# Optimization experiments

Hardware: AMD Instinct MI355X
Metric: run time of the kernel (lower is better)

Reference implementation:

```python
import jax, jax.numpy as jnp
import numpy as np
import math

N_HEAD = 16


def _alibi_slopes(n_head):
    def get_slopes(n):
        start = 2.0 ** (-2.0 ** (-(math.log2(n) - 3)))
        return [start * start ** i for i in range(n)]
    if math.log2(n_head).is_integer():
        slopes = get_slopes(n_head)
    else:
        c = 2 ** math.floor(math.log2(n_head))
        slopes = get_slopes(c)
        extra = get_slopes(2 * c)[0::2]
        slopes = slopes + extra[: n_head - c]
    return np.asarray(slopes, dtype=np.float32)


def setup_inputs() -> dict:
    key = jax.random.key(0)
    ks = jax.random.split(key, 9)
    B, S, E = 2, 2048, 1024
    sd = 1.0 / math.sqrt(E)
    inp = {
        "x": jax.random.normal(ks[0], (B, S, E), jnp.float32),
        "Wq": jax.random.uniform(ks[1], (E, E), jnp.float32, -sd, sd),
        "bq": jnp.zeros((E,), jnp.float32),
        "Wk": jax.random.uniform(ks[2], (E, E), jnp.float32, -sd, sd),
        "bk": jnp.zeros((E,), jnp.float32),
        "Wv": jax.random.uniform(ks[3], (E, E), jnp.float32, -sd, sd),
        "bv": jnp.zeros((E,), jnp.float32),
        "Wo": jax.random.uniform(ks[4], (E, E), jnp.float32, -sd, sd),
        "bo": jnp.zeros((E,), jnp.float32),
        "alibi_slopes": jnp.asarray(_alibi_slopes(N_HEAD)),
    }
    return inp


def reference(x, Wq, bq, Wk, bk, Wv, bv, Wo, bo, alibi_slopes):
    B, S, E = x.shape
    H = N_HEAD
    hd = E // H
    scale = hd ** -0.5
    # Linear layers (torch Linear: y = x @ W.T + b)
    Q = (x @ Wq.T + bq).reshape(B, H, S, hd)  # faithful: view, NOT transpose
    K = (x @ Wk.T + bk).reshape(B, H, S, hd)
    V = (x @ Wv.T + bv).reshape(B, H, S, hd)
    scores = jnp.einsum("bhqd,bhkd->bhqk", Q, K) * scale
    pos = jnp.arange(S)
    rel = jnp.abs(pos[None, :] - pos[:, None]).astype(scores.dtype)  # [S,S]
    bias = alibi_slopes[None, :, None, None] * rel[None, None]  # [1,H,S,S]
    scores = scores - bias
    probs = jax.nn.softmax(scores, axis=-1)
    # faithful quirk: keep only head index 1's probs, broadcast to all heads
    probs1 = probs[:, 1:2, :, :]  # [B,1,S,S]
    attn_out = jnp.matmul(probs1, V)  # broadcast -> [B,H,S,hd]
    attn_out = attn_out.reshape(B, S, E)
    out = attn_out @ Wo.T + bo
    return (out, probs1)
```

## Files before the change

### kernel.cpp

```cpp
#include <hip/hip_runtime.h>

typedef __bf16 bf16;
typedef __bf16 bf16_4 __attribute__((ext_vector_type(4)));
typedef __bf16 bf16_8 __attribute__((ext_vector_type(8)));
typedef float f32_4 __attribute__((ext_vector_type(4)));

#define GLDS16(g, l) \
  __builtin_amdgcn_global_load_lds((const __attribute__((address_space(1))) unsigned int*)(g), \
                                   (__attribute__((address_space(3))) unsigned int*)(l), 16, 0, 0)

__global__ __launch_bounds__(256) void convert_all(
    const float* __restrict__ x, const float* __restrict__ wq, const float* __restrict__ wk,
    const float* __restrict__ wv, const float* __restrict__ wo,
    bf16* __restrict__ xb, bf16* __restrict__ wqb, bf16* __restrict__ wkb,
    bf16* __restrict__ wvb, bf16* __restrict__ wob)
{
    for (int i = blockIdx.x * 256 + threadIdx.x; i < 2097152; i += 2048 * 256) {
        const float* s; bf16* d; int off;
        if (i < 1048576) { s = x; d = xb; off = i; }
        else {
            int j = i - 1048576;
            int sel = j >> 18;
            off = j & 262143;
            s = (sel == 0) ? wq : (sel == 1) ? wk : (sel == 2) ? wv : wo;
            d = (sel == 0) ? wqb : (sel == 1) ? wkb : (sel == 2) ? wvb : wob;
        }
        float4 v = reinterpret_cast<const float4*>(s)[off];
        bf16_4 o; o.x = (bf16)v.x; o.y = (bf16)v.y; o.z = (bf16)v.z; o.w = (bf16)v.w;
        reinterpret_cast<bf16_4*>(d)[off] = o;
    }
}

template<int BM, int KU>
__device__ __forceinline__ void gemm_core(
    const bf16* __restrict__ Ab, int lda,
    const bf16* __restrict__ Wb, int ldw,
    int K, int m0, int n0, int tid,
    bf16* As, bf16* Bs,
    f32_4 (&acc)[4][(BM == 128) ? 4 : 2])
{
    constexpr int NJ = (BM == 128) ? 4 : 2;
    constexpr int CA = BM * 8;
    const int lane = tid & 63;
    const int wave = tid >> 6;
    const int l15  = lane & 15;
    const int quad = lane >> 4;
    const int WM = (BM == 128) ? (wave >> 1) * 64 : 0;
    const int WN = (BM == 128) ? (wave & 1) * 64 : wave * 32;

#pragma unroll
    for (int i = 0; i < 4; i++)
#pragma unroll
        for (int j = 0; j < NJ; j++) acc[i][j] = (f32_4)(0.0f);

    for (int k0 = 0; k0 < K; k0 += 64 * KU) {
#pragma unroll
        for (int ku = 0; ku < KU; ++ku) {
            bf16* Asu = As + ku * BM * 64;
            bf16* Bsu = Bs + ku * 128 * 64;
            int kk = k0 + ku * 64;
#pragma unroll
            for (int it = 0; it < CA / 256; ++it) {
                int p = wave * (CA / 4) + it * 64 + lane;
                int r = p >> 3;
                int q = (p & 7) ^ (r & 7);
                GLDS16(Ab + (long long)(m0 + r) * lda + kk + q * 8, Asu + p * 8);
            }
#pragma unroll
            for (int it = 0; it < 4; ++it) {
                int p = wave * 256 + it * 64 + lane;
                int r = p >> 3;
                int q = (p & 7) ^ (r & 7);
                GLDS16(Wb + (long long)(n0 + r) * ldw + kk + q * 8, Bsu + p * 8);
            }
        }
        __syncthreads();

#pragma unroll
        for (int ku = 0; ku < KU; ++ku) {
            bf16* Asu = As + ku * BM * 64;
            bf16* Bsu = Bs + ku * 128 * 64;
#pragma unroll
            for (int kh = 0; kh < 2; ++kh) {
                bf16_8 af[4], bfr[NJ];
#pragma unroll
                for (int t = 0; t < 4; ++t) {
                    int r = WM + t * 16 + l15;
                    int q = (kh * 4 + quad) ^ (r & 7);
                    af[t] = *reinterpret_cast<const bf16_8*>(&Asu[r * 64 + q * 8]);
                }
#pragma unroll
                for (int j = 0; j < NJ; ++j) {
                    int r = WN + j * 16 + l15;
                    int q = (kh * 4 + quad) ^ (r & 7);
                    bfr[j] = *reinterpret_cast<const bf16_8*>(&Bsu[r * 64 + q * 8]);
                }
#pragma unroll
                for (int i = 0; i < 4; ++i)
#pragma unroll
                    for (int j = 0; j < NJ; ++j)
                        acc[i][j] = __builtin_amdgcn_mfma_f32_16x16x32_bf16(af[i], bfr[j], acc[i][j], 0, 0, 0);
            }
        }
        __syncthreads();
    }
}

__global__ __launch_bounds__(256) void proj_merged(
    const bf16* __restrict__ x_bf,
    const bf16* __restrict__ wv_bf, const float* __restrict__ bv, bf16* __restrict__ v_bf,
    const bf16* __restrict__ wq_bf, const float* __restrict__ bq, bf16* __restrict__ qh1,
    const bf16* __restrict__ wk_bf, const float* __restrict__ bk, bf16* __restrict__ kh1)
{
    __shared__ alignas(16) bf16 As[64 * 64 * 2];
    __shared__ alignas(16) bf16 Bs[128 * 64 * 2];
    const int tid = threadIdx.x;
    const int lane = tid & 63, wave = tid >> 6, l15 = lane & 15, quad = lane >> 4;
    const int n0 = blockIdx.x * 128;

    int m0;
    const bf16* Ab; const bf16* Wb; const float* bvec; bf16* op;
    long long obase;
    int y = blockIdx.y;
    if (y < 64) { m0 = y * 64; Ab = x_bf; Wb = wv_bf; bvec = bv; op = v_bf; obase = 0; }
    else {
        int sub = y - 64;
        int batch = (sub >> 1) & 1;
        int sel = sub >> 2;
        m0 = (sub & 1) * 64;
        Ab = x_bf + (long long)batch * 2097152LL + 131072LL;
        Wb = sel ? wk_bf : wq_bf;
        bvec = sel ? bk : bq;
        op = sel ? kh1 : qh1;
        obase = (long long)batch * 131072LL;
    }

    f32_4 acc[4][2];
    gemm_core<64, 2>(Ab, 1024, Wb, 1024, 1024, m0, n0, tid, As, Bs, acc);

    const int WN = wave * 32;
#pragma unroll
    for (int i = 0; i < 4; i++)
#pragma unroll
        for (int j = 0; j < 2; j++)
#pragma unroll
            for (int rg = 0; rg < 4; rg++) {
                int m = m0 + i * 16 + quad * 4 + rg;
                int n = n0 + WN + j * 16 + l15;
                op[obase + (long long)m * 1024 + n] = (bf16)(acc[i][j][rg] + bvec[n]);
            }
}

__global__ __launch_bounds__(256) void scores_tr(
    const bf16* __restrict__ qh1, const bf16* __restrict__ kh1,
    const float* __restrict__ slopes,
    bf16* __restrict__ pb, float* __restrict__ spart,
    const unsigned short* __restrict__ v_bf, unsigned short* __restrict__ vt)
{
    __shared__ alignas(16) char smem[32768];
    bf16* As = (bf16*)smem;
    bf16* Bs = (bf16*)(smem + 16384);
    const int tid = threadIdx.x;
    const int lane = tid & 63, wave = tid >> 6, l15 = lane & 15, quad = lane >> 4;
    const int n0 = blockIdx.x * 128;
    const int m0 = blockIdx.y * 128;
    const int z  = blockIdx.z;

    f32_4 acc[4][4];
    gemm_core<128, 1>(qh1 + (long long)z * 131072LL, 64,
                      kh1 + (long long)z * 131072LL, 64, 64, m0, n0, tid, As, Bs, acc);

    const int WM = (wave >> 1) * 64;
    const int WN = (wave & 1) * 64;
    const float slope = slopes[1];
    long long obase = (long long)z * 4194304LL;
#pragma unroll
    for (int i = 0; i < 4; i++) {
#pragma unroll
        for (int rg = 0; rg < 4; rg++) {
            int m = m0 + WM + i * 16 + quad * 4 + rg;
            float rowpart = 0.0f;
#pragma unroll
            for (int j = 0; j < 4; j++) {
                int n = n0 + WN + j * 16 + l15;
                float v = acc[i][j][rg] * 0.125f - slope * fabsf((float)(m - n));
                float e = __expf(v);
                rowpart += e;
                pb[obase + (long long)m * 2048 + n] = (bf16)e;
            }
            rowpart += __shfl_xor(rowpart, 1, 64);
            rowpart += __shfl_xor(rowpart, 2, 64);
            rowpart += __shfl_xor(rowpart, 4, 64);
            rowpart += __shfl_xor(rowpart, 8, 64);
            if (l15 == 0)
                spart[((long long)z * 2048 + m) * 32 + (n0 >> 6) + (WN >> 6)] = rowpart;
        }
    }

    unsigned short* tile = (unsigned short*)smem;
    int flat = z * 256 + blockIdx.y * 16 + blockIdx.x;
#pragma unroll
    for (int uu = 0; uu < 2; ++uu) {
        int u = flat * 2 + uu;
        int k0 = (u & 31) * 64, h = (u >> 5) & 15, b = u >> 9;
        const unsigned short* src = v_bf + (long long)b * 2097152LL + (long long)h * 131072LL;
#pragma unroll
        for (int p = 0; p < 8; p++) {
            int idx = tid + p * 256;
            int k = idx >> 5, dc = idx & 31;
            ushort2 w = *reinterpret_cast<const ushort2*>(&src[(long long)(k0 + k) * 64 + dc * 2]);
            tile[(dc * 2) * 66 + k]     = w.x;
            tile[(dc * 2 + 1) * 66 + k] = w.y;
        }
        __syncthreads();
        unsigned short* dst = vt + (long long)b * 2097152LL + (long long)h * 64 * 2048LL + k0;
#pragma unroll
        for (int p = 0; p < 8; p++) {
            int idx = tid + p * 256;
            int d = idx >> 5, kc = idx & 31;
            ushort2 w;
            w.x = tile[d * 66 + kc * 2];
            w.y = tile[d * 66 + kc * 2 + 1];
            *reinterpret_cast<ushort2*>(&dst[(long long)d * 2048 + kc * 2]) = w;
        }
        __syncthreads();
    }
}

__global__ __launch_bounds__(256) void pv_fused(
    const bf16* __restrict__ pb, const bf16* __restrict__ vt,
    const float* __restrict__ spart,
    bf16* __restrict__ attn, float* __restrict__ probs_f)
{
    __shared__ alignas(16) bf16 As[64 * 64 * 2];
    __shared__ alignas(16) bf16 Bs[128 * 64 * 2];
    __shared__ float rs[64];
    const int tid = threadIdx.x;
    const int lane = tid & 63, wave = tid >> 6, l15 = lane & 15, quad = lane >> 4;
    const int nx = blockIdx.x;
    const int n0 = nx * 128;
    const int m0 = blockIdx.y * 64;
    const int z  = blockIdx.z;

    {
        int r = tid >> 2, part = tid & 3;
        const float* sp = spart + ((long long)z * 2048 + m0 + r) * 32 + part * 8;
        float4 a = *reinterpret_cast<const float4*>(sp);
        float4 b = *reinterpret_cast<const float4*>(sp + 4);
        float v = a.x + a.y + a.z + a.w + b.x + b.y + b.z + b.w;
        v += __shfl_xor(v, 1, 64);
        v += __shfl_xor(v, 2, 64);
        if (part == 0) rs[r] = 1.0f / v;
    }
    __syncthreads();

    const bf16* Ab = pb + (long long)z * 4194304LL;
    const bf16* Wb = vt + (long long)z * 2097152LL;

    f32_4 acc[4][2];
#pragma unroll
    for (int i = 0; i < 4; i++)
#pragma unroll
        for (int j = 0; j < 2; j++) acc[i][j] = (f32_4)(0.0f);

    for (int k0 = 0; k0 < 2048; k0 += 128) {
#pragma unroll
        for (int ku = 0; ku < 2; ++ku) {
            bf16* Asu = As + ku * 4096;
            bf16* Bsu = Bs + ku * 8192;
            int kk = k0 + ku * 64;
#pragma unroll
            for (int it = 0; it < 2; ++it) {
                int p = wave * 128 + it * 64 + lane;
                int r = p >> 3, q = (p & 7) ^ (r & 7);
                GLDS16(Ab + (long long)(m0 + r) * 2048 + kk + q * 8, Asu + p * 8);
            }
#pragma unroll
            for (int it = 0; it < 4; ++it) {
                int p = wave * 256 + it * 64 + lane;
                int r = p >> 3, q = (p & 7) ^ (r & 7);
                GLDS16(Wb + (long long)(n0 + r) * 2048 + kk + q * 8, Bsu + p * 8);
            }
        }
        __syncthreads();

#pragma unroll
        for (int ku = 0; ku < 2; ++ku) {
            int kk = k0 + ku * 64;
            if ((kk >> 8) == nx) {
                bf16* Asu = As + ku * 4096;
#pragma unroll
                for (int s0 = 0; s0 < 2; ++s0) {
                    int s = tid + s0 * 256;
                    int r = s >> 3, q = s & 7;
                    bf16_8 e = *reinterpret_cast<const bf16_8*>(&Asu[r * 64 + (q ^ (r & 7)) * 8]);
                    float inv = rs[r];
                    float4 o0, o1;
                    o0.x = (float)e[0] * inv; o0.y = (float)e[1] * inv;
                    o0.z = (float)e[2] * inv; o0.w = (float)e[3] * inv;
                    o1.x = (float)e[4] * inv; o1.y = (float)e[5] * inv;
                    o1.z = (float)e[6] * inv; o1.w = (float)e[7] * inv;
                    long long base = ((long long)z * 2048 + m0 + r) * 2048 + kk + q * 8;
                    *reinterpret_cast<float4*>(&probs_f[base])     = o0;
                    *reinterpret_cast<float4*>(&probs_f[base + 4]) = o1;
                }
            }
        }

#pragma unroll
        for (int ku = 0; ku < 2; ++ku) {
            bf16* Asu = As + ku * 4096;
            bf16* Bsu = Bs + ku * 8192;
#pragma unroll
            for (int kh = 0; kh < 2; ++kh) {
                bf16_8 af[4], bfr[2];
#pragma unroll
                for (int t = 0; t < 4; ++t) {
                    int r = t * 16 + l15;
                    int q = (kh * 4 + quad) ^ (r & 7);
                    af[t] = *reinterpret_cast<const bf16_8*>(&Asu[r * 64 + q * 8]);
                }
                const int WN = wave * 32;
#pragma unroll
                for (int j = 0; j < 2; ++j) {
                    int r = WN + j * 16 + l15;
                    int q = (kh * 4 + quad) ^ (r & 7);
                    bfr[j] = *reinterpret_cast<const bf16_8*>(&Bsu[r * 64 + q * 8]);
                }
#pragma unroll
                for (int i = 0; i < 4; ++i)
#pragma unroll
                    for (int j = 0; j < 2; ++j)
                        acc[i][j] = __builtin_amdgcn_mfma_f32_16x16x32_bf16(af[i], bfr[j], acc[i][j], 0, 0, 0);
            }
        }
        __syncthreads();
    }

    const int WN = wave * 32;
    long long obase = (long long)z * 2097152LL;
#pragma unroll
    for (int i = 0; i < 4; i++)
#pragma unroll
        for (int j = 0; j < 2; j++)
#pragma unroll
            for (int rg = 0; rg < 4; rg++) {
                int ml = i * 16 + quad * 4 + rg;
                int m = m0 + ml;
                int n = n0 + WN + j * 16 + l15;
                float v = acc[i][j][rg] * rs[ml];
                long long off = obase + ((long long)(n >> 6)) * 131072LL + (long long)m * 64 + (n & 63);
                attn[off] = (bf16)v;
            }
}

__global__ __launch_bounds__(256) void out_proj(
    const bf16* __restrict__ attn, const bf16* __restrict__ wo_bf,
    const float* __restrict__ bo, float* __restrict__ out_f)
{
    __shared__ alignas(16) bf16 As[64 * 64 * 2];
    __shared__ alignas(16) bf16 Bs[128 * 64 * 2];
    const int tid = threadIdx.x;
    const int lane = tid & 63, wave = tid >> 6, l15 = lane & 15, quad = lane >> 4;
    const int n0 = blockIdx.x * 128;
    const int m0 = blockIdx.y * 64;

    f32_4 acc[4][2];
    gemm_core<64, 2>(attn, 1024, wo_bf, 1024, 1024, m0, n0, tid, As, Bs, acc);

    const int WN = wave * 32;
#pragma unroll
    for (int i = 0; i < 4; i++)
#pragma unroll
        for (int j = 0; j < 2; j++)
#pragma unroll
            for (int rg = 0; rg < 4; rg++) {
                int m = m0 + i * 16 + quad * 4 + rg;
                int n = n0 + WN + j * 16 + l15;
                out_f[(long long)m * 1024 + n] = acc[i][j][rg] + bo[n];
            }
}

extern "C" void kernel_launch(void* const* d_in, const int* in_sizes, int n_in,
                              void* d_out, int out_size, void* d_ws, size_t ws_size,
                              hipStream_t stream) {
    const float* x      = (const float*)d_in[0];
    const float* Wq     = (const float*)d_in[1];
    const float* bq     = (const float*)d_in[2];
    const float* Wk     = (const float*)d_in[3];
    const float* bk     = (const float*)d_in[4];
    const float* Wv     = (const float*)d_in[5];
    const float* bv     = (const float*)d_in[6];
    const float* Wo     = (const float*)d_in[7];
    const float* bo     = (const float*)d_in[8];
    const float* slopes = (const float*)d_in[9];

    char* w = (char*)d_ws;
    bf16* x_bf  = (bf16*)w;  w += 4096LL * 1024 * 2;
    bf16* wq_bf = (bf16*)w;  w += 1024LL * 1024 * 2;
    bf16* wk_bf = (bf16*)w;  w += 1024LL * 1024 * 2;
    bf16* wv_bf = (bf16*)w;  w += 1024LL * 1024 * 2;
    bf16* wo_bf = (bf16*)w;  w += 1024LL * 1024 * 2;
    bf16* qh1   = (bf16*)w;  w += 2LL * 131072 * 2;
    bf16* kh1   = (bf16*)w;  w += 2LL * 131072 * 2;
    bf16* v_bf  = (bf16*)w;  w += 4096LL * 1024 * 2;
    bf16* vt    = (bf16*)w;  w += 2LL * 1024 * 2048 * 2;
    bf16* attn  = (bf16*)w;  w += 4096LL * 1024 * 2;
    bf16* pb    = (bf16*)w;  w += 2LL * 2048 * 2048 * 2;
    float* spart = (float*)w; w += 4096LL * 32 * 4;

    float* out_f   = (float*)d_out;
    float* probs_f = (float*)d_out + 4194304LL;

    convert_all<<<2048, 256, 0, stream>>>(x, Wq, Wk, Wv, Wo, x_bf, wq_bf, wk_bf, wv_bf, wo_bf);

    proj_merged<<<dim3(8, 72, 1), 256, 0, stream>>>(
        x_bf, wv_bf, bv, v_bf, wq_bf, bq, qh1, wk_bf, bk, kh1);

    scores_tr<<<dim3(16, 16, 2), 256, 0, stream>>>(
        qh1, kh1, slopes, pb, spart,
        (const unsigned short*)v_bf, (unsigned short*)vt);

    pv_fused<<<dim3(8, 32, 2), 256, 0, stream>>>(pb, vt, spart, attn, probs_f);

    out_proj<<<dim3(8, 64, 1), 256, 0, stream>>>(attn, wo_bf, bo, out_f);
}
```

Before: 177.0 us.

## Double-buffer and enlarge tiles to 128x128 in PV and output projection GEMMs

```diff
diff --git a/kernel.cpp b/kernel.cpp
--- a/kernel.cpp
+++ b/kernel.cpp
@@ -103,6 +103,60 @@
             }
         }
         __syncthreads();
+    }
+}
+
+__device__ __forceinline__ void stage128(
+    const bf16* __restrict__ Ab, long long lda,
+    const bf16* __restrict__ Wb, long long ldw,
+    int m0, int n0, int kk0, int wave, int lane,
+    bf16* Asb, bf16* Bsb)
+{
+#pragma unroll
+    for (int ku = 0; ku < 2; ++ku) {
+        bf16* Asu = Asb + ku * 8192;
+        bf16* Bsu = Bsb + ku * 8192;
+        int kk = kk0 + ku * 64;
+#pragma unroll
+        for (int it = 0; it < 4; ++it) {
+            int p = wave * 256 + it * 64 + lane;
+            int r = p >> 3, q = (p & 7) ^ (r & 7);
+            GLDS16(Ab + (long long)(m0 + r) * lda + kk + q * 8, Asu + p * 8);
+            GLDS16(Wb + (long long)(n0 + r) * ldw + kk + q * 8, Bsu + p * 8);
+        }
+    }
+}
+
+__device__ __forceinline__ void mma128(
+    const bf16* Asb, const bf16* Bsb,
+    int WM, int WN, int l15, int quad,
+    f32_4 (&acc)[4][4])
+{
+#pragma unroll
+    for (int ku = 0; ku < 2; ++ku) {
+        const bf16* Asu = Asb + ku * 8192;
+        const bf16* Bsu = Bsb + ku * 8192;
+#pragma unroll
+        for (int kh = 0; kh < 2; ++kh) {
+            bf16_8 af[4], bfr[4];
+#pragma unroll
+            for (int t = 0; t < 4; ++t) {
+                int r = WM + t * 16 + l15;
+                int q = (kh * 4 + quad) ^ (r & 7);
+                af[t] = *reinterpret_cast<const bf16_8*>(&Asu[r * 64 + q * 8]);
+            }
+#pragma unroll
+            for (int j = 0; j < 4; ++j) {
+                int r = WN + j * 16 + l15;
+                int q = (kh * 4 + quad) ^ (r & 7);
+                bfr[j] = *reinterpret_cast<const bf16_8*>(&Bsu[r * 64 + q * 8]);
+            }
+#pragma unroll
+            for (int i = 0; i < 4; ++i)
+#pragma unroll
+                for (int j = 0; j < 4; ++j)
+                    acc[i][j] = __builtin_amdgcn_mfma_f32_16x16x32_bf16(af[i], bfr[j], acc[i][j], 0, 0, 0);
+        }
     }
 }
 
@@ -232,65 +286,60 @@
     const float* __restrict__ spart,
     bf16* __restrict__ attn, float* __restrict__ probs_f)
 {
-    __shared__ alignas(16) bf16 As[64 * 64 * 2];
-    __shared__ alignas(16) bf16 Bs[128 * 64 * 2];
-    __shared__ float rs[64];
+    __shared__ alignas(16) bf16 As[2][16384];
+    __shared__ alignas(16) bf16 Bs[2][16384];
+    __shared__ float rs[128];
     const int tid = threadIdx.x;
     const int lane = tid & 63, wave = tid >> 6, l15 = lane & 15, quad = lane >> 4;
     const int nx = blockIdx.x;
     const int n0 = nx * 128;
-    const int m0 = blockIdx.y * 64;
+    const int m0 = blockIdx.y * 128;
     const int z  = blockIdx.z;
+    const int WM = (wave >> 1) * 64, WN = (wave & 1) * 64;
+
+    const bf16* Ab = pb + (long long)z * 4194304LL;
+    const bf16* Wb = vt + (long long)z * 2097152LL;
+
+    stage128(Ab, 2048, Wb, 2048, m0, n0, 0, wave, lane, &As[0][0], &Bs[0][0]);
 
     {
-        int r = tid >> 2, part = tid & 3;
-        const float* sp = spart + ((long long)z * 2048 + m0 + r) * 32 + part * 8;
+        int r = tid >> 1, part = tid & 1;
+        const float* sp = spart + ((long long)z * 2048 + m0 + r) * 32 + part * 16;
         float4 a = *reinterpret_cast<const float4*>(sp);
         float4 b = *reinterpret_cast<const float4*>(sp + 4);
-        float v = a.x + a.y + a.z + a.w + b.x + b.y + b.z + b.w;
+        float4 c = *reinterpret_cast<const float4*>(sp + 8);
+        float4 d = *reinterpret_cast<const float4*>(sp + 12);
+        float v = a.x + a.y + a.z + a.w + b.x + b.y + b.z + b.w
+                + c.x + c.y + c.z + c.w + d.x + d.y + d.z + d.w;
         v += __shfl_xor(v, 1, 64);
-        v += __shfl_xor(v, 2, 64);
         if (part == 0) rs[r] = 1.0f / v;
     }
     __syncthreads();
 
-    const bf16* Ab = pb + (long long)z * 4194304LL;
-    const bf16* Wb = vt + (long long)z * 2097152LL;
-
-    f32_4 acc[4][2];
-#pragma unroll
-    for (int i = 0; i < 4; i++)
-#pragma unroll
-        for (int j = 0; j < 2; j++) acc[i][j] = (f32_4)(0.0f);
-
-    for (int k0 = 0; k0 < 2048; k0 += 128) {
+    f32_4 acc[4][4];
+#pragma unroll
+    for (int i = 0; i < 4; i++)
+#pragma unroll
+        for (int j = 0; j < 4; j++) acc[i][j] = (f32_4)(0.0f);
+
+    for (int t = 0; t < 16; ++t) {
+        const int cur = t & 1;
+        if (t < 15) {
+            stage128(Ab, 2048, Wb, 2048, m0, n0, (t + 1) * 128, wave, lane,
+                     &As[cur ^ 1][0], &Bs[cur ^ 1][0]);
+            asm volatile("s_waitcnt vmcnt(16)" ::: "memory");
+        } else {
+            asm volatile("s_waitcnt vmcnt(0)" ::: "memory");
+        }
+        __builtin_amdgcn_s_barrier();
+
 #pragma unroll
         for (int ku = 0; ku < 2; ++ku) {
-            bf16* Asu = As + ku * 4096;
-            bf16* Bsu = Bs + ku * 8192;
-            int kk = k0 + ku * 64;
-#pragma unroll
-            for (int it = 0; it < 2; ++it) {
-                int p = wave * 128 + it * 64 + lane;
-                int r = p >> 3, q = (p & 7) ^ (r & 7);
-                GLDS16(Ab + (long long)(m0 + r) * 2048 + kk + q * 8, Asu + p * 8);
-            }
-#pragma unroll
-            for (int it = 0; it < 4; ++it) {
-                int p = wave * 256 + it * 64 + lane;
-                int r = p >> 3, q = (p & 7) ^ (r & 7);
-                GLDS16(Wb + (long long)(n0 + r) * 2048 + kk + q * 8, Bsu + p * 8);
-            }
-        }
-        __syncthreads();
-
-#pragma unroll
-        for (int ku = 0; ku < 2; ++ku) {
-            int kk = k0 + ku * 64;
+            int kk = t * 128 + ku * 64;
             if ((kk >> 8) == nx) {
-                bf16* Asu = As + ku * 4096;
-#pragma unroll
-                for (int s0 = 0; s0 < 2; ++s0) {
+                const bf16* Asu = &As[cur][ku * 8192];
+#pragma unroll
+                for (int s0 = 0; s0 < 4; ++s0) {
                     int s = tid + s0 * 256;
                     int r = s >> 3, q = s & 7;
                     bf16_8 e = *reinterpret_cast<const bf16_8*>(&Asu[r * 64 + (q ^ (r & 7)) * 8]);
@@ -307,45 +356,20 @@
             }
         }
 
-#pragma unroll
-        for (int ku = 0; ku < 2; ++ku) {
-            bf16* Asu = As + ku * 4096;
-            bf16* Bsu = Bs + ku * 8192;
-#pragma unroll
-            for (int kh = 0; kh < 2; ++kh) {
-                bf16_8 af[4], bfr[2];
-#pragma unroll
-                for (int t = 0; t < 4; ++t) {
-                    int r = t * 16 + l15;
-                    int q = (kh * 4 + quad) ^ (r & 7);
-                    af[t] = *reinterpret_cast<const bf16_8*>(&Asu[r * 64 + q * 8]);
-                }
-                const int WN = wave * 32;
-#pragma unroll
-                for (int j = 0; j < 2; ++j) {
-                    int r = WN + j * 16 + l15;
-                    int q = (kh * 4 + quad) ^ (r & 7);
-                    bfr[j] = *reinterpret_cast<const bf16_8*>(&Bsu[r * 64 + q * 8]);
-                }
-#pragma unroll
-                for (int i = 0; i < 4; ++i)
-#pragma unroll
-                    for (int j = 0; j < 2; ++j)
-                        acc[i][j] = __builtin_amdgcn_mfma_f32_16x16x32_bf16(af[i], bfr[j], acc[i][j], 0, 0, 0);
-            }
-        }
-        __syncthreads();
-    }
-
-    const int WN = wave * 32;
+        mma128(&As[cur][0], &Bs[cur][0], WM, WN, l15, quad, acc);
+
+        asm volatile("s_waitcnt lgkmcnt(0)" ::: "memory");
+        __builtin_amdgcn_s_barrier();
+    }
+
     long long obase = (long long)z * 2097152LL;
 #pragma unroll
     for (int i = 0; i < 4; i++)
 #pragma unroll
-        for (int j = 0; j < 2; j++)
+        for (int j = 0; j < 4; j++)
 #pragma unroll
             for (int rg = 0; rg < 4; rg++) {
-                int ml = i * 16 + quad * 4 + rg;
+                int ml = WM + i * 16 + quad * 4 + rg;
                 int m = m0 + ml;
                 int n = n0 + WN + j * 16 + l15;
                 float v = acc[i][j][rg] * rs[ml];
@@ -358,24 +382,47 @@
     const bf16* __restrict__ attn, const bf16* __restrict__ wo_bf,
     const float* __restrict__ bo, float* __restrict__ out_f)
 {
-    __shared__ alignas(16) bf16 As[64 * 64 * 2];
-    __shared__ alignas(16) bf16 Bs[128 * 64 * 2];
+    __shared__ alignas(16) bf16 As[2][16384];
+    __shared__ alignas(16) bf16 Bs[2][16384];
     const int tid = threadIdx.x;
     const int lane = tid & 63, wave = tid >> 6, l15 = lane & 15, quad = lane >> 4;
     const int n0 = blockIdx.x * 128;
-    const int m0 = blockIdx.y * 64;
-
-    f32_4 acc[4][2];
-    gemm_core<64, 2>(attn, 1024, wo_bf, 1024, 1024, m0, n0, tid, As, Bs, acc);
-
-    const int WN = wave * 32;
-#pragma unroll
-    for (int i = 0; i < 4; i++)
-#pragma unroll
-        for (int j = 0; j < 2; j++)
+    const int m0 = blockIdx.y * 128;
+    const int WM = (wave >> 1) * 64, WN = (wave & 1) * 64;
+
+    stage128(attn, 1024, wo_bf, 1024, m0, n0, 0, wave, lane, &As[0][0], &Bs[0][0]);
+    __syncthreads();
+
+    f32_4 acc[4][4];
+#pragma unroll
+    for (int i = 0; i < 4; i++)
+#pragma unroll
+        for (int j = 0; j < 4; j++) acc[i][j] = (f32_4)(0.0f);
+
+    for (int t = 0; t < 8; ++t) {
+        const int cur = t & 1;
+        if (t < 7) {
+            stage128(attn, 1024, wo_bf, 1024, m0, n0, (t + 1) * 128, wave, lane,
+                     &As[cur ^ 1][0], &Bs[cur ^ 1][0]);
+            asm volatile("s_waitcnt vmcnt(16)" ::: "memory");
+        } else {
+            asm volatile("s_waitcnt vmcnt(0)" ::: "memory");
+        }
+        __builtin_amdgcn_s_barrier();
+
+        mma128(&As[cur][0], &Bs[cur][0], WM, WN, l15, quad, acc);
+
+        asm volatile("s_waitcnt lgkmcnt(0)" ::: "memory");
+        __builtin_amdgcn_s_barrier();
+    }
+
+#pragma unroll
+    for (int i = 0; i < 4; i++)
+#pragma unroll
+        for (int j = 0; j < 4; j++)
 #pragma unroll
             for (int rg = 0; rg < 4; rg++) {
-                int m = m0 + i * 16 + quad * 4 + rg;
+                int m = m0 + WM + i * 16 + quad * 4 + rg;
                 int n = n0 + WN + j * 16 + l15;
                 out_f[(long long)m * 1024 + n] = acc[i][j][rg] + bo[n];
             }
@@ -421,7 +468,7 @@
         qh1, kh1, slopes, pb, spart,
         (const unsigned short*)v_bf, (unsigned short*)vt);
 
-    pv_fused<<<dim3(8, 32, 2), 256, 0, stream>>>(pb, vt, spart, attn, probs_f);
-
-    out_proj<<<dim3(8, 64, 1), 256, 0, stream>>>(attn, wo_bf, bo, out_f);
-}
+    pv_fused<<<dim3(8, 16, 2), 256, 0, stream>>>(pb, vt, spart, attn, probs_f);
+
+    out_proj<<<dim3(8, 32, 1), 256, 0, stream>>>(attn, wo_bf, bo, out_f);
+}
```

New measurement: 186.9 us. +5.6%, slower.
